# Performance work log

Measured on AMD Instinct MI355X. Metric: run time of the kernel, lower is better.

## Reference

```python
import jax, jax.numpy as jnp
import numpy as np

N = 100000
E = 3200000
IN_F = 256
OUT_F = 128
ALPHA = 0.2  # LeakyReLU negative slope


def setup_inputs() -> dict:
    key = jax.random.key(0)
    k1, k2, k3, k4, k5 = jax.random.split(key, 5)
    x = jax.random.normal(k1, (N, IN_F), dtype=jnp.float32)
    edge_row = jax.random.randint(k2, (E,), 0, N, dtype=jnp.int32)
    edge_col = jax.random.randint(k3, (E,), 0, N, dtype=jnp.int32)
    # xavier-uniform style scaling (gain 1.414)
    lim_W = 1.414 * np.sqrt(6.0 / (IN_F + OUT_F))
    W = jax.random.uniform(k4, (IN_F, OUT_F), minval=-lim_W, maxval=lim_W, dtype=jnp.float32)
    lim_a = 1.414 * np.sqrt(6.0 / (1 + 2 * OUT_F))
    a = jax.random.uniform(k5, (2 * OUT_F,), minval=-lim_a, maxval=lim_a, dtype=jnp.float32)
    return {"x": x, "edge_row": edge_row, "edge_col": edge_col, "W": W, "a": a}


def reference(x, edge_row, edge_col, W, a):
    # h = x @ W : [N, OUT_F]
    h = x @ W
    # edge score: leakyrelu([h_src || h_dst] . a) computed as two node-level dots
    a_src, a_dst = a[:OUT_F], a[OUT_F:]
    s_src = h @ a_src  # [N]
    s_dst = h @ a_dst  # [N]
    e = s_src[edge_row] + s_dst[edge_col]  # [E]
    e = jnp.where(e > 0, e, ALPHA * e)     # LeakyReLU
    # sparse softmax along dim=1 (over columns within each row -> segment by row)
    row_max = jax.ops.segment_max(e, edge_row, num_segments=N)  # [N]
    e_exp = jnp.exp(e - row_max[edge_row])
    row_sum = jax.ops.segment_sum(e_exp, edge_row, num_segments=N)  # [N]
    att = e_exp / row_sum[edge_row]  # [E]
    # sparse-dense matmul: h_prime[i] = sum_j att_ij * h[j]
    h_prime = jax.ops.segment_sum(att[:, None] * h[edge_col], edge_row, num_segments=N)
    # concat=True -> ELU
    return jax.nn.elu(h_prime)
```

## Files before the change

### kernel.cpp

```cpp
#include <hip/hip_runtime.h>
#include <math.h>

#define N_NODES 100000
#define N_EDGES 3200000
#define IN_FEAT 256
#define OUT_FEAT 128
#define ALPHA 0.2f
#define NB 782
#define NBLK 200
#define CHUNK 16000

#define SCAN_N (NB * NBLK)
#define SCAN_ELEMS 2048
#define SCAN_BLOCKS ((SCAN_N + SCAN_ELEMS - 1) / SCAN_ELEMS)

typedef __attribute__((ext_vector_type(8))) short short8;
typedef __attribute__((ext_vector_type(4))) float f32x4;

__device__ __forceinline__ ushort f2bf(float f) {
  uint u = __float_as_uint(f);
  u = (u + 0x7FFFu + ((u >> 16) & 1u)) >> 16;
  return (ushort)u;
}
__device__ __forceinline__ float bflo(uint u) { return __uint_as_float(u << 16); }
__device__ __forceinline__ float bfhi(uint u) { return __uint_as_float(u & 0xFFFF0000u); }

__global__ __launch_bounds__(256) void wt_kernel(const float* __restrict__ W,
                                                 ushort* __restrict__ Wt) {
  int id = blockIdx.x * 256 + threadIdx.x;
  int c = id >> 8;
  int k = id & 255;
  Wt[id] = f2bf(W[k * OUT_FEAT + c]);
}

#define GBM 128
#define GBK 32
#define A_LD 40
#define C_LD 136

__global__ __launch_bounds__(256) void gemm_h16_kernel(const float* __restrict__ x,
                                                       const ushort* __restrict__ Wt,
                                                       ushort* __restrict__ h16) {
  __shared__ union {
    struct { ushort A[GBM * A_LD]; ushort B[OUT_FEAT * A_LD]; } s;
    ushort C[GBM * C_LD];
  } sm;
  const int tid = threadIdx.x;
  const int row0 = blockIdx.x * GBM;
  const int lane = tid & 63;
  const int wave = tid >> 6;
  const int lr = lane & 15;
  const int lg = lane >> 4;

  f32x4 acc[2][8];
#pragma unroll
  for (int m = 0; m < 2; ++m)
#pragma unroll
    for (int n = 0; n < 8; ++n) acc[m][n] = (f32x4)(0.f);

  const int sr = tid >> 1;
  const int sh = tid & 1;
  const bool arow_ok = (row0 + sr) < N_NODES;
  const float* xg = x + (size_t)(row0 + sr) * IN_FEAT + sh * 16;
  const ushort* wg = Wt + sr * IN_FEAT + sh * 16;

  for (int ks = 0; ks < IN_FEAT / GBK; ++ks) {
    float4 f[4];
    if (arow_ok) {
#pragma unroll
      for (int i = 0; i < 4; ++i) f[i] = *(const float4*)(xg + ks * GBK + i * 4);
    } else {
#pragma unroll
      for (int i = 0; i < 4; ++i) f[i] = make_float4(0.f, 0.f, 0.f, 0.f);
    }
#pragma unroll
    for (int i = 0; i < 4; ++i) {
      uint2 p;
      p.x = (uint)f2bf(f[i].x) | ((uint)f2bf(f[i].y) << 16);
      p.y = (uint)f2bf(f[i].z) | ((uint)f2bf(f[i].w) << 16);
      *(uint2*)&sm.s.A[sr * A_LD + sh * 16 + i * 4] = p;
    }
    {
      short8 b0 = *(const short8*)(wg + ks * GBK);
      short8 b1 = *(const short8*)(wg + ks * GBK + 8);
      *(short8*)&sm.s.B[sr * A_LD + sh * 16] = b0;
      *(short8*)&sm.s.B[sr * A_LD + sh * 16 + 8] = b1;
    }
    __syncthreads();
    short8 af[2], bf[8];
#pragma unroll
    for (int m = 0; m < 2; ++m)
      af[m] = *(const short8*)&sm.s.A[(wave * 32 + m * 16 + lr) * A_LD + lg * 8];
#pragma unroll
    for (int n = 0; n < 8; ++n)
      bf[n] = *(const short8*)&sm.s.B[(n * 16 + lr) * A_LD + lg * 8];
#pragma unroll
    for (int m = 0; m < 2; ++m)
#pragma unroll
      for (int n = 0; n < 8; ++n)
        acc[m][n] = __builtin_amdgcn_mfma_f32_16x16x32_bf16(af[m], bf[n], acc[m][n], 0, 0, 0);
    __syncthreads();
  }

#pragma unroll
  for (int m = 0; m < 2; ++m)
#pragma unroll
    for (int n = 0; n < 8; ++n)
#pragma unroll
      for (int i = 0; i < 4; ++i)
        sm.C[(wave * 32 + m * 16 + lg * 4 + i) * C_LD + n * 16 + lr] = f2bf(acc[m][n][i]);
  __syncthreads();
  {
    int row = tid >> 1;
    if (row0 + row < N_NODES) {
      const ushort* src = &sm.C[row * C_LD + sh * 64];
      ushort* dst = h16 + (size_t)(row0 + row) * OUT_FEAT + sh * 64;
#pragma unroll
      for (int i = 0; i < 8; ++i) *(short8*)(dst + i * 8) = *(const short8*)(src + i * 8);
    }
  }
}

__global__ __launch_bounds__(256) void s16_kernel(const ushort* __restrict__ h16,
                                                  const float* __restrict__ a,
                                                  float* __restrict__ s_src,
                                                  float* __restrict__ s_dst) {
  const int lane = threadIdx.x & 63;
  const int r = blockIdx.x * 4 + (threadIdx.x >> 6);
  uint v = *(const uint*)(h16 + (size_t)r * OUT_FEAT + lane * 2);
  float h0 = bflo(v);
  float h1 = bfhi(v);
  float2 as = *(const float2*)(a + lane * 2);
  float2 ad = *(const float2*)(a + OUT_FEAT + lane * 2);
  float ds = h0 * as.x + h1 * as.y;
  float dd = h0 * ad.x + h1 * ad.y;
#pragma unroll
  for (int off = 32; off >= 1; off >>= 1) {
    ds += __shfl_xor(ds, off, 64);
    dd += __shfl_xor(dd, off, 64);
  }
  if (lane == 0) {
    s_src[r] = ds;
    s_dst[r] = dd;
  }
}

__global__ __launch_bounds__(256) void hist_kernel(const int* __restrict__ erow,
                                                   int* __restrict__ G) {
  __shared__ int hist[NB];
  const int b = blockIdx.x;
  const int t = threadIdx.x;
  for (int k = t; k < NB; k += 256) hist[k] = 0;
  __syncthreads();
  const int base = b * CHUNK;
  for (int i = base + t; i < base + CHUNK; i += 256) atomicAdd(&hist[erow[i] >> 7], 1);
  __syncthreads();
  for (int k = t; k < NB; k += 256) G[k * NBLK + b] = hist[k];
}

__global__ __launch_bounds__(256) void scan1_kernel(const int* __restrict__ src,
                                                    int* __restrict__ dst,
                                                    int* __restrict__ bsum) {
  __shared__ int tsum[256];
  const int b = blockIdx.x;
  const int t = threadIdx.x;
  const int base = b * SCAN_ELEMS + t * 8;
  int v[8];
  int s = 0;
#pragma unroll
  for (int i = 0; i < 8; ++i) {
    int idx = base + i;
    v[i] = (idx < SCAN_N) ? src[idx] : 0;
    s += v[i];
  }
  tsum[t] = s;
  __syncthreads();
  for (int d = 1; d < 256; d <<= 1) {
    int u = (t >= d) ? tsum[t - d] : 0;
    __syncthreads();
    tsum[t] += u;
    __syncthreads();
  }
  int run = (t == 0) ? 0 : tsum[t - 1];
#pragma unroll
  for (int i = 0; i < 8; ++i) {
    int idx = base + i;
    if (idx < SCAN_N) dst[idx] = run;
    run += v[i];
  }
  if (t == 255) bsum[b] = tsum[255];
}

__global__ __launch_bounds__(128) void scan2_kernel(int* __restrict__ bsum,
                                                    int* __restrict__ boff) {
  __shared__ int s[128];
  const int t = threadIdx.x;
  s[t] = (t < SCAN_BLOCKS) ? bsum[t] : 0;
  __syncthreads();
  for (int d = 1; d < 128; d <<= 1) {
    int u = (t >= d) ? s[t - d] : 0;
    __syncthreads();
    s[t] += u;
    __syncthreads();
  }
  boff[t + 1] = s[t];
  if (t == 0) boff[0] = 0;
}

__global__ __launch_bounds__(256) void scan3_kernel(int* __restrict__ dst,
                                                    const int* __restrict__ boff) {
  const int b = blockIdx.x;
  const int t = threadIdx.x;
  const int add = boff[b];
  const int base = b * SCAN_ELEMS + t * 8;
#pragma unroll
  for (int i = 0; i < 8; ++i) {
    int idx = base + i;
    if (idx < SCAN_N) dst[idx] += add;
  }
  if (b == 0 && t == 0) dst[SCAN_N] = boff[SCAN_BLOCKS];
}

__global__ __launch_bounds__(256) void partition_kernel(const int* __restrict__ erow,
                                                        const int* __restrict__ ecol,
                                                        const int* __restrict__ scanG,
                                                        uint* __restrict__ packed) {
  __shared__ int cur[NB];
  const int b = blockIdx.x;
  const int t = threadIdx.x;
  for (int k = t; k < NB; k += 256) cur[k] = scanG[k * NBLK + b];
  __syncthreads();
  const int base = b * CHUNK;
  for (int i = base + t; i < base + CHUNK; i += 256) {
    int r = erow[i];
    int c = ecol[i];
    int pos = atomicAdd(&cur[r >> 7], 1);
    packed[pos] = ((uint)(r & 127) << 17) | (uint)c;
  }
}

__global__ __launch_bounds__(256) void bucket_scatter_kernel(const uint* __restrict__ packed,
                                                             const int* __restrict__ scanG,
                                                             int* __restrict__ offs,
                                                             int* __restrict__ scol) {
  __shared__ int cnt[128];
  __shared__ int sc[128];
  const int b = blockIdx.x;
  const int t = threadIdx.x;
  const int beg = scanG[b * NBLK];
  const int end = scanG[(b + 1) * NBLK];
  if (t < 128) cnt[t] = 0;
  __syncthreads();
  for (int i = beg + t; i < end; i += 256) atomicAdd(&cnt[packed[i] >> 17], 1);
  __syncthreads();
  if (t < 128) sc[t] = cnt[t];
  __syncthreads();
  for (int d = 1; d < 128; d <<= 1) {
    int v = 0;
    if (t >= d && t < 128) v = sc[t - d];
    __syncthreads();
    if (t < 128) sc[t] += v;
    __syncthreads();
  }
  const int row0 = b << 7;
  if (t < 128) {
    int rstart = beg + sc[t] - cnt[t];
    if (row0 + t < N_NODES) offs[row0 + t] = rstart;
    sc[t] = rstart;
    cnt[t] = 0;
  }
  if (b == NB - 1 && t == 0) offs[N_NODES] = end;
  __syncthreads();
  for (int i = beg + t; i < end; i += 256) {
    uint p = packed[i];
    int rl = p >> 17;
    int pos = sc[rl] + atomicAdd(&cnt[rl], 1);
    scol[pos] = (int)(p & 0x1FFFFu);
  }
}

__global__ __launch_bounds__(256) void attn_kernel(const ushort* __restrict__ h16,
                                                   const float* __restrict__ s_src,
                                                   const float* __restrict__ s_dst,
                                                   const int* __restrict__ offs,
                                                   const int* __restrict__ scol,
                                                   float* __restrict__ out) {
  const int lane = threadIdx.x & 63;
  const int r = blockIdx.x * 4 + (threadIdx.x >> 6);
  const int o0 = offs[r];
  const int deg = offs[r + 1] - o0;
  const int sl = lane & 31;
  const int half = lane >> 5;
  float* orow = out + (size_t)r * OUT_FEAT + sl * 4;

  if (deg == 0) {
    if (half == 0) *(float4*)orow = make_float4(0.f, 0.f, 0.f, 0.f);
    return;
  }

  const float ssrc = s_src[r];
  const ushort* hb = h16 + sl * 4;
  float acc0 = 0.f, acc1 = 0.f, acc2 = 0.f, acc3 = 0.f;

  if (deg <= 128) {
    int c0 = 0, c1 = 0;
    float p0 = -INFINITY, p1 = -INFINITY;
    if (lane < deg) {
      c0 = scol[o0 + lane];
      float e = ssrc + s_dst[c0];
      p0 = e > 0.f ? e : ALPHA * e;
    }
    if (lane + 64 < deg) {
      c1 = scol[o0 + 64 + lane];
      float e = ssrc + s_dst[c1];
      p1 = e > 0.f ? e : ALPHA * e;
    }
    float m = fmaxf(p0, p1);
#pragma unroll
    for (int off = 32; off >= 1; off >>= 1) m = fmaxf(m, __shfl_xor(m, off, 64));
    p0 = __expf(p0 - m);
    p1 = __expf(p1 - m);
    float ssum = p0 + p1;
#pragma unroll
    for (int off = 32; off >= 1; off >>= 1) ssum += __shfl_xor(ssum, off, 64);
    const float inv = 1.f / ssum;
    p0 *= inv;
    p1 *= inv;

    const int d0 = deg < 64 ? deg : 64;
    const int d0e = d0 & ~1;
    for (int j = 0; j < d0e; j += 2) {
      int jj = j + half;
      float att = __shfl(p0, jj, 64);
      int c = __shfl(c0, jj, 64);
      uint2 v = *(const uint2*)(hb + (size_t)c * OUT_FEAT);
      acc0 = fmaf(att, bflo(v.x), acc0);
      acc1 = fmaf(att, bfhi(v.x), acc1);
      acc2 = fmaf(att, bflo(v.y), acc2);
      acc3 = fmaf(att, bfhi(v.y), acc3);
    }
    if (d0 & 1) {
      float attv = __shfl(p0, d0e, 64);
      int c = __shfl(c0, d0e, 64);
      float att = half ? 0.f : attv;
      uint2 v = *(const uint2*)(hb + (size_t)c * OUT_FEAT);
      acc0 = fmaf(att, bflo(v.x), acc0);
      acc1 = fmaf(att, bfhi(v.x), acc1);
      acc2 = fmaf(att, bflo(v.y), acc2);
      acc3 = fmaf(att, bfhi(v.y), acc3);
    }
    if (deg > 64) {
      const int d1 = deg - 64;
      const int d1e = d1 & ~1;
      for (int j = 0; j < d1e; j += 2) {
        int jj = j + half;
        float att = __shfl(p1, jj, 64);
        int c = __shfl(c1, jj, 64);
        uint2 v = *(const uint2*)(hb + (size_t)c * OUT_FEAT);
        acc0 = fmaf(att, bflo(v.x), acc0);
        acc1 = fmaf(att, bfhi(v.x), acc1);
        acc2 = fmaf(att, bflo(v.y), acc2);
        acc3 = fmaf(att, bfhi(v.y), acc3);
      }
      if (d1 & 1) {
        float attv = __shfl(p1, d1e, 64);
        int c = __shfl(c1, d1e, 64);
        float att = half ? 0.f : attv;
        uint2 v = *(const uint2*)(hb + (size_t)c * OUT_FEAT);
        acc0 = fmaf(att, bflo(v.x), acc0);
        acc1 = fmaf(att, bfhi(v.x), acc1);
        acc2 = fmaf(att, bflo(v.y), acc2);
        acc3 = fmaf(att, bfhi(v.y), acc3);
      }
    }
  } else {
    float m = -INFINITY;
    for (int j = lane; j < deg; j += 64) {
      int c = scol[o0 + j];
      float e = ssrc + s_dst[c];
      e = e > 0.f ? e : ALPHA * e;
      m = fmaxf(m, e);
    }
#pragma unroll
    for (int off = 32; off >= 1; off >>= 1) m = fmaxf(m, __shfl_xor(m, off, 64));
    float ssum = 0.f;
    for (int j = lane; j < deg; j += 64) {
      int c = scol[o0 + j];
      float e = ssrc + s_dst[c];
      e = e > 0.f ? e : ALPHA * e;
      ssum += __expf(e - m);
    }
#pragma unroll
    for (int off = 32; off >= 1; off >>= 1) ssum += __shfl_xor(ssum, off, 64);
    const float inv = 1.f / ssum;
    for (int j = 0; j < deg; j += 2) {
      int jj = j + half;
      float att = 0.f;
      int c = 0;
      if (jj < deg) {
        c = scol[o0 + jj];
        float e = ssrc + s_dst[c];
        e = e > 0.f ? e : ALPHA * e;
        att = __expf(e - m) * inv;
      }
      uint2 v = *(const uint2*)(hb + (size_t)c * OUT_FEAT);
      acc0 = fmaf(att, bflo(v.x), acc0);
      acc1 = fmaf(att, bfhi(v.x), acc1);
      acc2 = fmaf(att, bflo(v.y), acc2);
      acc3 = fmaf(att, bfhi(v.y), acc3);
    }
  }

  acc0 += __shfl_xor(acc0, 32, 64);
  acc1 += __shfl_xor(acc1, 32, 64);
  acc2 += __shfl_xor(acc2, 32, 64);
  acc3 += __shfl_xor(acc3, 32, 64);
  if (half == 0) {
    acc0 = acc0 > 0.f ? acc0 : expm1f(acc0);
    acc1 = acc1 > 0.f ? acc1 : expm1f(acc1);
    acc2 = acc2 > 0.f ? acc2 : expm1f(acc2);
    acc3 = acc3 > 0.f ? acc3 : expm1f(acc3);
    *(float4*)orow = make_float4(acc0, acc1, acc2, acc3);
  }
}

extern "C" void kernel_launch(void* const* d_in, const int* in_sizes, int n_in,
                              void* d_out, int out_size, void* d_ws, size_t ws_size,
                              hipStream_t stream) {
  const float* x = (const float*)d_in[0];
  const int* erow = (const int*)d_in[1];
  const int* ecol = (const int*)d_in[2];
  const float* W = (const float*)d_in[3];
  const float* a = (const float*)d_in[4];
  float* out = (float*)d_out;

  char* ws = (char*)d_ws;
  size_t off = 0;
  auto alloc = [&](size_t bytes) {
    void* p = ws + off;
    off = (off + bytes + 255) & ~(size_t)255;
    return p;
  };
  const int M_PAD = 782 * GBM;
  ushort* h16 = (ushort*)alloc((size_t)M_PAD * OUT_FEAT * sizeof(ushort));
  ushort* Wt = (ushort*)alloc((size_t)IN_FEAT * OUT_FEAT * sizeof(ushort));
  float* s_src = (float*)alloc((size_t)N_NODES * sizeof(float));
  float* s_dst = (float*)alloc((size_t)N_NODES * sizeof(float));
  int* offs = (int*)alloc((size_t)(N_NODES + 1) * sizeof(int));
  int* G = (int*)alloc((size_t)SCAN_N * sizeof(int));
  int* scanG = (int*)alloc((size_t)(SCAN_N + 1) * sizeof(int));
  int* bsum = (int*)alloc((size_t)SCAN_BLOCKS * sizeof(int));
  int* boff = (int*)alloc((size_t)(SCAN_BLOCKS + 64) * sizeof(int));
  uint* packed = (uint*)alloc((size_t)N_EDGES * sizeof(uint));
  int* scol = (int*)alloc((size_t)N_EDGES * sizeof(int));

  wt_kernel<<<(IN_FEAT * OUT_FEAT) / 256, 256, 0, stream>>>(W, Wt);
  gemm_h16_kernel<<<782, 256, 0, stream>>>(x, Wt, h16);
  s16_kernel<<<N_NODES / 4, 256, 0, stream>>>(h16, a, s_src, s_dst);
  hist_kernel<<<NBLK, 256, 0, stream>>>(erow, G);
  scan1_kernel<<<SCAN_BLOCKS, 256, 0, stream>>>(G, scanG, bsum);
  scan2_kernel<<<1, 128, 0, stream>>>(bsum, boff);
  scan3_kernel<<<SCAN_BLOCKS, 256, 0, stream>>>(scanG, boff);
  partition_kernel<<<NBLK, 256, 0, stream>>>(erow, ecol, scanG, packed);
  bucket_scatter_kernel<<<NB, 256, 0, stream>>>(packed, scanG, offs, scol);
  attn_kernel<<<N_NODES / 4, 256, 0, stream>>>(h16, s_src, s_dst, offs, scol, out);
}
```

Baseline: 265.5 us.

## Gather four neighbors per wave with 16-byte loads and LDS-staged attention pairs

Restructures the attention aggregation so each wave processes four edges at a time, with 16 lanes each loading 8 bf16 features via uint4 loads instead of two edges with 32 lanes loading uint2. Attention weights and column indices are staged in shared memory as pairs, replacing per-iteration shuffles with LDS reads. Degree is padded to a multiple of four using padded entries with zero weight and column 0. The goal is fewer loop iterations and wider memory transactions for the gather, at the cost of more registers and an extra cross-group reduction step.

```diff
diff --git a/kernel.cpp b/kernel.cpp
--- a/kernel.cpp
+++ b/kernel.cpp
@@ -285,22 +285,27 @@
                                                    const int* __restrict__ offs,
                                                    const int* __restrict__ scol,
                                                    float* __restrict__ out) {
+  __shared__ uint2 apair[4][128];
   const int lane = threadIdx.x & 63;
-  const int r = blockIdx.x * 4 + (threadIdx.x >> 6);
+  const int w = threadIdx.x >> 6;
+  const int r = blockIdx.x * 4 + w;
   const int o0 = offs[r];
   const int deg = offs[r + 1] - o0;
-  const int sl = lane & 31;
-  const int half = lane >> 5;
-  float* orow = out + (size_t)r * OUT_FEAT + sl * 4;
+  const int g = lane >> 4;
+  const int fo = (lane & 15) * 8;
+  float* orow = out + (size_t)r * OUT_FEAT + fo;
 
   if (deg == 0) {
-    if (half == 0) *(float4*)orow = make_float4(0.f, 0.f, 0.f, 0.f);
+    if (g == 0) {
+      *(float4*)orow = make_float4(0.f, 0.f, 0.f, 0.f);
+      *(float4*)(orow + 4) = make_float4(0.f, 0.f, 0.f, 0.f);
+    }
     return;
   }
 
   const float ssrc = s_src[r];
-  const ushort* hb = h16 + sl * 4;
-  float acc0 = 0.f, acc1 = 0.f, acc2 = 0.f, acc3 = 0.f;
+  const ushort* hb = h16 + fo;
+  float acc[8] = {0.f, 0.f, 0.f, 0.f, 0.f, 0.f, 0.f, 0.f};
 
   if (deg <= 128) {
     int c0 = 0, c1 = 0;
@@ -327,51 +332,23 @@
     p0 *= inv;
     p1 *= inv;
 
-    const int d0 = deg < 64 ? deg : 64;
-    const int d0e = d0 & ~1;
-    for (int j = 0; j < d0e; j += 2) {
-      int jj = j + half;
-      float att = __shfl(p0, jj, 64);
-      int c = __shfl(c0, jj, 64);
-      uint2 v = *(const uint2*)(hb + (size_t)c * OUT_FEAT);
-      acc0 = fmaf(att, bflo(v.x), acc0);
-      acc1 = fmaf(att, bfhi(v.x), acc1);
-      acc2 = fmaf(att, bflo(v.y), acc2);
-      acc3 = fmaf(att, bfhi(v.y), acc3);
-    }
-    if (d0 & 1) {
-      float attv = __shfl(p0, d0e, 64);
-      int c = __shfl(c0, d0e, 64);
-      float att = half ? 0.f : attv;
-      uint2 v = *(const uint2*)(hb + (size_t)c * OUT_FEAT);
-      acc0 = fmaf(att, bflo(v.x), acc0);
-      acc1 = fmaf(att, bfhi(v.x), acc1);
-      acc2 = fmaf(att, bflo(v.y), acc2);
-      acc3 = fmaf(att, bfhi(v.y), acc3);
-    }
-    if (deg > 64) {
-      const int d1 = deg - 64;
-      const int d1e = d1 & ~1;
-      for (int j = 0; j < d1e; j += 2) {
-        int jj = j + half;
-        float att = __shfl(p1, jj, 64);
-        int c = __shfl(c1, jj, 64);
-        uint2 v = *(const uint2*)(hb + (size_t)c * OUT_FEAT);
-        acc0 = fmaf(att, bflo(v.x), acc0);
-        acc1 = fmaf(att, bfhi(v.x), acc1);
-        acc2 = fmaf(att, bflo(v.y), acc2);
-        acc3 = fmaf(att, bfhi(v.y), acc3);
-      }
-      if (d1 & 1) {
-        float attv = __shfl(p1, d1e, 64);
-        int c = __shfl(c1, d1e, 64);
-        float att = half ? 0.f : attv;
-        uint2 v = *(const uint2*)(hb + (size_t)c * OUT_FEAT);
-        acc0 = fmaf(att, bflo(v.x), acc0);
-        acc1 = fmaf(att, bfhi(v.x), acc1);
-        acc2 = fmaf(att, bflo(v.y), acc2);
-        acc3 = fmaf(att, bfhi(v.y), acc3);
-      }
+    apair[w][lane] = make_uint2(__float_as_uint(p0), (uint)c0);
+    apair[w][64 + lane] = make_uint2(__float_as_uint(p1), (uint)c1);
+
+    const int degR = (deg + 3) & ~3;
+#pragma unroll 2
+    for (int j = 0; j < degR; j += 4) {
+      uint2 pr = apair[w][j + g];
+      float att = __uint_as_float(pr.x);
+      uint4 v = *(const uint4*)(hb + (size_t)pr.y * OUT_FEAT);
+      acc[0] = fmaf(att, bflo(v.x), acc[0]);
+      acc[1] = fmaf(att, bfhi(v.x), acc[1]);
+      acc[2] = fmaf(att, bflo(v.y), acc[2]);
+      acc[3] = fmaf(att, bfhi(v.y), acc[3]);
+      acc[4] = fmaf(att, bflo(v.z), acc[4]);
+      acc[5] = fmaf(att, bfhi(v.z), acc[5]);
+      acc[6] = fmaf(att, bflo(v.w), acc[6]);
+      acc[7] = fmaf(att, bfhi(v.w), acc[7]);
     }
   } else {
     float m = -INFINITY;
@@ -393,8 +370,8 @@
 #pragma unroll
     for (int off = 32; off >= 1; off >>= 1) ssum += __shfl_xor(ssum, off, 64);
     const float inv = 1.f / ssum;
-    for (int j = 0; j < deg; j += 2) {
-      int jj = j + half;
+    for (int j = 0; j < deg; j += 4) {
+      int jj = j + g;
       float att = 0.f;
       int c = 0;
       if (jj < deg) {
@@ -403,24 +380,28 @@
         e = e > 0.f ? e : ALPHA * e;
         att = __expf(e - m) * inv;
       }
-      uint2 v = *(const uint2*)(hb + (size_t)c * OUT_FEAT);
-      acc0 = fmaf(att, bflo(v.x), acc0);
-      acc1 = fmaf(att, bfhi(v.x), acc1);
-      acc2 = fmaf(att, bflo(v.y), acc2);
-      acc3 = fmaf(att, bfhi(v.y), acc3);
-    }
-  }
-
-  acc0 += __shfl_xor(acc0, 32, 64);
-  acc1 += __shfl_xor(acc1, 32, 64);
-  acc2 += __shfl_xor(acc2, 32, 64);
-  acc3 += __shfl_xor(acc3, 32, 64);
-  if (half == 0) {
-    acc0 = acc0 > 0.f ? acc0 : expm1f(acc0);
-    acc1 = acc1 > 0.f ? acc1 : expm1f(acc1);
-    acc2 = acc2 > 0.f ? acc2 : expm1f(acc2);
-    acc3 = acc3 > 0.f ? acc3 : expm1f(acc3);
-    *(float4*)orow = make_float4(acc0, acc1, acc2, acc3);
+      uint4 v = *(const uint4*)(hb + (size_t)c * OUT_FEAT);
+      acc[0] = fmaf(att, bflo(v.x), acc[0]);
+      acc[1] = fmaf(att, bfhi(v.x), acc[1]);
+      acc[2] = fmaf(att, bflo(v.y), acc[2]);
+      acc[3] = fmaf(att, bfhi(v.y), acc[3]);
+      acc[4] = fmaf(att, bflo(v.z), acc[4]);
+      acc[5] = fmaf(att, bfhi(v.z), acc[5]);
+      acc[6] = fmaf(att, bflo(v.w), acc[6]);
+      acc[7] = fmaf(att, bfhi(v.w), acc[7]);
+    }
+  }
+
+#pragma unroll
+  for (int k = 0; k < 8; ++k) {
+    acc[k] += __shfl_xor(acc[k], 16, 64);
+    acc[k] += __shfl_xor(acc[k], 32, 64);
+  }
+  if (g == 0) {
+#pragma unroll
+    for (int k = 0; k < 8; ++k) acc[k] = acc[k] > 0.f ? acc[k] : expm1f(acc[k]);
+    *(float4*)orow = make_float4(acc[0], acc[1], acc[2], acc[3]);
+    *(float4*)(orow + 4) = make_float4(acc[4], acc[5], acc[6], acc[7]);
   }
 }
 
```

Result: faster. 242.3 us (-8.7%).
